# Kernel tuning notes

Hardware: AMD Instinct MI355X
Metric: run time of the kernel (lower is better)

Reference implementation:

```python
import jax, jax.numpy as jnp
import numpy as np

NUM_SKILLS = 1000
DIM_S = 64
SIZE_M = 64
B, T = 64, 200


def setup_inputs() -> dict:
    key = jax.random.key(0)
    ks = jax.random.split(key, 16)
    skills = jax.random.randint(ks[0], (B, T), 0, NUM_SKILLS)
    responses = jax.random.randint(ks[1], (B, T), 0, 2)
    s = 1.0 / np.sqrt(DIM_S)
    return {
        "skills": skills,
        "responses": responses,
        "k_emb": jax.random.normal(ks[2], (NUM_SKILLS, DIM_S)) * s,
        "v_emb": jax.random.normal(ks[3], (2 * NUM_SKILLS, DIM_S)) * s,
        "Mk": jax.random.normal(ks[4], (SIZE_M, DIM_S)) * np.sqrt(2.0 / DIM_S),
        "Mv0": jax.random.normal(ks[5], (SIZE_M, DIM_S)) * np.sqrt(2.0 / DIM_S),
        "fW": jax.random.normal(ks[6], (DIM_S, 2 * DIM_S)) * (1.0 / np.sqrt(2 * DIM_S)),
        "fb": jnp.zeros((DIM_S,)),
        "eW": jax.random.normal(ks[7], (DIM_S, DIM_S)) * s,
        "eb": jnp.zeros((DIM_S,)),
        "aW": jax.random.normal(ks[8], (DIM_S, DIM_S)) * s,
        "ab": jnp.zeros((DIM_S,)),
        "pW": jax.random.normal(ks[9], (1, DIM_S)) * s,
        "pb": jnp.zeros((1,)),
    }


def reference(skills, responses, k_emb, v_emb, Mk, Mv0, fW, fb, eW, eb, aW, ab, pW, pb):
    # dropout is identity in eval mode
    masked_r = responses * (responses > -1).astype(responses.dtype)
    x = skills + NUM_SKILLS * masked_r            # [B, T]
    k = k_emb[skills]                              # [B, T, D]
    v = v_emb[x]                                   # [B, T, D]
    w = jax.nn.softmax(jnp.einsum('btd,md->btm', k, Mk), axis=-1)  # [B, T, M]
    e = jax.nn.sigmoid(v @ eW.T + eb)              # [B, T, D]
    a = jnp.tanh(v @ aW.T + ab)                    # [B, T, D]

    Mv_init = jnp.broadcast_to(Mv0, (skills.shape[0],) + Mv0.shape)  # [B, M, D]

    def step(Mvt, inp):
        wt, et, at = inp                           # [B,M], [B,D], [B,D]
        read = jnp.einsum('bm,bmd->bd', wt, Mvt)   # read BEFORE update (Mv[:, :-1])
        Mvt = Mvt * (1.0 - wt[:, :, None] * et[:, None, :]) + wt[:, :, None] * at[:, None, :]
        return Mvt, read

    xs = (jnp.swapaxes(w, 0, 1), jnp.swapaxes(e, 0, 1), jnp.swapaxes(a, 0, 1))
    _, reads = jax.lax.scan(step, Mv_init, xs)     # reads: [T, B, D]
    reads = jnp.swapaxes(reads, 0, 1)              # [B, T, D]

    f = jnp.tanh(jnp.concatenate([reads, k], axis=-1) @ fW.T + fb)  # [B, T, D]
    p = jax.nn.sigmoid(f @ pW.T + pb)[..., 0]      # [B, T]
    return p[:, 1:]                                # pred, [B, T-1]
```

## Files before the change

### kernel.cpp

```cpp
#include <hip/hip_runtime.h>
#include <hip/hip_bf16.h>
#include <stdint.h>

#define NSK 1000
#define DD 64
#define MM 64
#define BB 64
#define TT 200

__device__ __forceinline__ float lane_bcast(float v, int l) {
  return __uint_as_float(__builtin_amdgcn_readlane(__float_as_uint(v), l));
}

__global__ __launch_bounds__(256) void wea_kernel(
    const int* __restrict__ skills, const int* __restrict__ responses,
    const float* __restrict__ k_emb, const float* __restrict__ v_emb,
    const float* __restrict__ Mk, const float* __restrict__ eW,
    const float* __restrict__ eb, const float* __restrict__ aW,
    const float* __restrict__ ab,
    float* __restrict__ w_ws, float* __restrict__ e_ws, float* __restrict__ a_ws)
{
  __shared__ float sMk[4096], seW[4096], saW[4096];
  const int tid = threadIdx.x;
  for (int Q = tid; Q < 1024; Q += 256) {
    const int j = Q >> 4, c = Q & 15;
    const int dst = j * 64 + ((c + j) & 15) * 4;
    *(float4*)&sMk[dst] = ((const float4*)Mk)[Q];
    *(float4*)&seW[dst] = ((const float4*)eW)[Q];
    *(float4*)&saW[dst] = ((const float4*)aW)[Q];
  }
  __syncthreads();

  const int wave = tid >> 6, lane = tid & 63;
  const float ebl = eb[lane], abl = ab[lane];

  float kvs[4], vvs[4];
  #pragma unroll
  for (int i = 0; i < 4; ++i) {
    const int row = blockIdx.x * 16 + wave * 4 + i;
    const int sk = skills[row];
    int r = responses[row]; r = (r > -1) ? r : 0;
    kvs[i] = k_emb[(size_t)sk * DD + lane];
    vvs[i] = v_emb[(size_t)(sk + NSK * r) * DD + lane];
  }

  #pragma unroll 1
  for (int i = 0; i < 4; ++i) {
    const int row = blockIdx.x * 16 + wave * 4 + i;
    const float kv = kvs[i], vv = vvs[i];

    float accK = 0.f, accE = 0.f, accA = 0.f;
    #pragma unroll
    for (int c = 0; c < 16; ++c) {
      const int off = lane * 64 + ((c + lane) & 15) * 4;
      float4 qm = *(const float4*)&sMk[off];
      float4 qe = *(const float4*)&seW[off];
      float4 qa = *(const float4*)&saW[off];
      float mm[4] = {qm.x, qm.y, qm.z, qm.w};
      float ee[4] = {qe.x, qe.y, qe.z, qe.w};
      float aa[4] = {qa.x, qa.y, qa.z, qa.w};
      #pragma unroll
      for (int j = 0; j < 4; ++j) {
        const int d = c * 4 + j;
        const float kd = lane_bcast(kv, d);
        const float vd = lane_bcast(vv, d);
        accK = fmaf(kd, mm[j], accK);
        accE = fmaf(vd, ee[j], accE);
        accA = fmaf(vd, aa[j], accA);
      }
    }
    float mx = accK;
    #pragma unroll
    for (int off = 32; off; off >>= 1) mx = fmaxf(mx, __shfl_xor(mx, off));
    float ex = __expf(accK - mx);
    float sm = ex;
    #pragma unroll
    for (int off = 32; off; off >>= 1) sm += __shfl_xor(sm, off);
    const float wv  = ex / sm;
    const float evv = 1.f / (1.f + __expf(-(accE + ebl)));
    const float avv = tanhf(accA + abl);
    w_ws[(size_t)row * 64 + lane] = wv;
    e_ws[(size_t)row * 64 + lane] = evv;
    a_ws[(size_t)row * 64 + lane] = avv;
  }
}

#define CH 8

__device__ __forceinline__ void load_chunk(
    const float* __restrict__ wr, const float* __restrict__ er,
    const float* __restrict__ ar, int t0, int wl, int lane,
    float* wb, float* ebf, float* abf)
{
  #pragma unroll
  for (int k = 0; k < CH; ++k) {
    wb[k]  = wr[(t0 + k) * 64 + wl];
    ebf[k] = er[(t0 + k) * 64 + lane];
    abf[k] = ar[(t0 + k) * 64 + lane];
  }
}

__device__ __forceinline__ void compute_chunk(
    float* Mv, const float* wb, const float* ebf, const float* abf,
    int t0, int wave, int lane, float* __restrict__ pr)
{
  #pragma unroll
  for (int k = 0; k < CH; ++k) {
    const float wv = wb[k], ev = ebf[k], av = abf[k];
    float rp = 0.f;
    #pragma unroll
    for (int i = 0; i < 16; ++i) {
      float wm = lane_bcast(wv, i);
      rp = fmaf(wm, Mv[i], rp);
      float tp = fmaf(-ev, Mv[i], av);
      Mv[i] = fmaf(wm, tp, Mv[i]);
    }
    pr[(t0 + k) * 256 + wave * 64 + lane] = rp;
  }
}

__global__ __launch_bounds__(256) void scan_kernel(
    const float* __restrict__ Mv0,
    const float* __restrict__ w_ws, const float* __restrict__ e_ws,
    const float* __restrict__ a_ws, float* __restrict__ part_ws)
{
  const int b    = blockIdx.x;
  const int wave = threadIdx.x >> 6;
  const int lane = threadIdx.x & 63;
  const int m0   = wave * 16;
  const int wl   = m0 + (lane & 15);
  float Mv[16];
  #pragma unroll
  for (int i = 0; i < 16; ++i) Mv[i] = Mv0[(size_t)(m0 + i) * DD + lane];

  const float* wr = w_ws + (size_t)b * TT * 64;
  const float* er = e_ws + (size_t)b * TT * 64;
  const float* ar = a_ws + (size_t)b * TT * 64;
  float* pr = part_ws + (size_t)b * TT * 256;

  float wb0[CH], eb0[CH], ab0[CH];
  float wb1[CH], eb1[CH], ab1[CH];
  load_chunk(wr, er, ar, 0, wl, lane, wb0, eb0, ab0);

  for (int ch = 0; ch < TT / CH; ch += 2) {
    if ((ch + 1) * CH < TT)
      load_chunk(wr, er, ar, (ch + 1) * CH, wl, lane, wb1, eb1, ab1);
    compute_chunk(Mv, wb0, eb0, ab0, ch * CH, wave, lane, pr);
    if ((ch + 2) * CH < TT)
      load_chunk(wr, er, ar, (ch + 2) * CH, wl, lane, wb0, eb0, ab0);
    if ((ch + 1) * CH < TT)
      compute_chunk(Mv, wb1, eb1, ab1, (ch + 1) * CH, wave, lane, pr);
  }
}

__global__ __launch_bounds__(256) void fp_kernel(
    const int* __restrict__ skills, const float* __restrict__ k_emb,
    const float* __restrict__ fW, const float* __restrict__ fb,
    const float* __restrict__ pW, const float* __restrict__ pb,
    const float* __restrict__ part_ws, float* __restrict__ out)
{
  __shared__ float sfW[8192];
  const int tid = threadIdx.x;
  for (int Q = tid; Q < 2048; Q += 256) {
    const int j = Q >> 5, c = Q & 31;
    *(float4*)&sfW[j * 128 + ((c + j) & 31) * 4] = ((const float4*)fW)[Q];
  }
  __syncthreads();

  const int wave = tid >> 6, lane = tid & 63;
  const float fbl = fb[lane];
  const float pwl = pW[lane];
  const float pb0 = pb[0];

  float rvs[4], kvs[4];
  #pragma unroll
  for (int i = 0; i < 4; ++i) {
    const int idx = blockIdx.x * 16 + wave * 4 + i;
    const int b   = idx / (TT - 1);
    const int tm1 = idx % (TT - 1);
    const int row = b * TT + tm1 + 1;
    const float* pp = part_ws + (size_t)row * 256;
    rvs[i] = (pp[lane] + pp[64 + lane]) + (pp[128 + lane] + pp[192 + lane]);
    kvs[i] = k_emb[(size_t)skills[row] * DD + lane];
  }

  #pragma unroll 1
  for (int i = 0; i < 4; ++i) {
    const int idx = blockIdx.x * 16 + wave * 4 + i;
    const int b   = idx / (TT - 1);
    const int tm1 = idx % (TT - 1);
    const float rv = rvs[i], kv = kvs[i];

    float acc = fbl;
    #pragma unroll
    for (int c = 0; c < 32; ++c) {
      const int off = lane * 128 + ((c + lane) & 31) * 4;
      float4 q = *(const float4*)&sfW[off];
      float ww[4] = {q.x, q.y, q.z, q.w};
      #pragma unroll
      for (int j = 0; j < 4; ++j) {
        const int d = c * 4 + j;
        const float s = (d < 64) ? lane_bcast(rv, d) : lane_bcast(kv, d - 64);
        acc = fmaf(s, ww[j], acc);
      }
    }
    float fj = tanhf(acc);
    float prod = fj * pwl;
    #pragma unroll
    for (int off = 32; off; off >>= 1) prod += __shfl_xor(prod, off);
    float p = 1.f / (1.f + __expf(-(prod + pb0)));
    if (lane == 0) out[(size_t)b * (TT - 1) + tm1] = p;
  }
}

extern "C" void kernel_launch(void* const* d_in, const int* in_sizes, int n_in,
                              void* d_out, int out_size, void* d_ws, size_t ws_size,
                              hipStream_t stream) {
  const int* skills    = (const int*)d_in[0];
  const int* responses = (const int*)d_in[1];
  const float* k_emb   = (const float*)d_in[2];
  const float* v_emb   = (const float*)d_in[3];
  const float* Mk      = (const float*)d_in[4];
  const float* Mv0     = (const float*)d_in[5];
  const float* fW      = (const float*)d_in[6];
  const float* fb      = (const float*)d_in[7];
  const float* eW      = (const float*)d_in[8];
  const float* eb      = (const float*)d_in[9];
  const float* aW      = (const float*)d_in[10];
  const float* ab      = (const float*)d_in[11];
  const float* pW      = (const float*)d_in[12];
  const float* pb      = (const float*)d_in[13];

  float* w_ws    = (float*)d_ws;
  float* e_ws    = w_ws + (size_t)BB * TT * 64;
  float* a_ws    = e_ws + (size_t)BB * TT * 64;
  float* part_ws = a_ws + (size_t)BB * TT * 64;

  wea_kernel<<<dim3(BB * TT / 16), 256, 0, stream>>>(
      skills, responses, k_emb, v_emb, Mk, eW, eb, aW, ab, w_ws, e_ws, a_ws);
  scan_kernel<<<dim3(BB), 256, 0, stream>>>(Mv0, w_ws, e_ws, a_ws, part_ws);
  fp_kernel<<<dim3(BB * (TT - 1) / 16), 256, 0, stream>>>(
      skills, k_emb, fW, fb, pW, pb, part_ws, (float*)d_out);
}
```

Baseline: 146.5 us.

## Split scan across two blocks per batch and reuse LDS weight loads across rows

The recurrent scan now runs on 128 blocks, two per batch, each owning 32 memory slots with 8 rows per wave instead of 16. This halves the serial per-step work per wave and doubles the number of CUs in use. The partial-read workspace grows to 8 partials per step, and fp_kernel sums all eight. Both wea_kernel and fp_kernel are also restructured so each LDS weight fragment is loaded once and applied to all 4 rows, reducing LDS traffic at the cost of more live registers. The larger partial buffer adds global write and read traffic.

```diff
diff --git a/kernel.cpp b/kernel.cpp
--- a/kernel.cpp
+++ b/kernel.cpp
@@ -44,48 +44,58 @@
     vvs[i] = v_emb[(size_t)(sk + NSK * r) * DD + lane];
   }
 
+  float accK[4] = {0.f, 0.f, 0.f, 0.f};
+  float accE[4] = {0.f, 0.f, 0.f, 0.f};
+  float accA[4] = {0.f, 0.f, 0.f, 0.f};
   #pragma unroll 1
+  for (int h = 0; h < 4; ++h) {
+    float4 qm[4], qe[4], qa[4];
+    #pragma unroll
+    for (int c = 0; c < 4; ++c) {
+      const int cc = h * 4 + c;
+      const int off = lane * 64 + ((cc + lane) & 15) * 4;
+      qm[c] = *(const float4*)&sMk[off];
+      qe[c] = *(const float4*)&seW[off];
+      qa[c] = *(const float4*)&saW[off];
+    }
+    #pragma unroll
+    for (int i = 0; i < 4; ++i) {
+      #pragma unroll
+      for (int c = 0; c < 4; ++c) {
+        const float mm[4] = {qm[c].x, qm[c].y, qm[c].z, qm[c].w};
+        const float ee[4] = {qe[c].x, qe[c].y, qe[c].z, qe[c].w};
+        const float aa[4] = {qa[c].x, qa[c].y, qa[c].z, qa[c].w};
+        #pragma unroll
+        for (int j = 0; j < 4; ++j) {
+          const int d = (h * 4 + c) * 4 + j;
+          const float kd = lane_bcast(kvs[i], d);
+          const float vd = lane_bcast(vvs[i], d);
+          accK[i] = fmaf(kd, mm[j], accK[i]);
+          accE[i] = fmaf(vd, ee[j], accE[i]);
+          accA[i] = fmaf(vd, aa[j], accA[i]);
+        }
+      }
+    }
+  }
+
+  #pragma unroll
   for (int i = 0; i < 4; ++i) {
     const int row = blockIdx.x * 16 + wave * 4 + i;
-    const float kv = kvs[i], vv = vvs[i];
-
-    float accK = 0.f, accE = 0.f, accA = 0.f;
-    #pragma unroll
-    for (int c = 0; c < 16; ++c) {
-      const int off = lane * 64 + ((c + lane) & 15) * 4;
-      float4 qm = *(const float4*)&sMk[off];
-      float4 qe = *(const float4*)&seW[off];
-      float4 qa = *(const float4*)&saW[off];
-      float mm[4] = {qm.x, qm.y, qm.z, qm.w};
-      float ee[4] = {qe.x, qe.y, qe.z, qe.w};
-      float aa[4] = {qa.x, qa.y, qa.z, qa.w};
-      #pragma unroll
-      for (int j = 0; j < 4; ++j) {
-        const int d = c * 4 + j;
-        const float kd = lane_bcast(kv, d);
-        const float vd = lane_bcast(vv, d);
-        accK = fmaf(kd, mm[j], accK);
-        accE = fmaf(vd, ee[j], accE);
-        accA = fmaf(vd, aa[j], accA);
-      }
-    }
-    float mx = accK;
+    float mx = accK[i];
     #pragma unroll
     for (int off = 32; off; off >>= 1) mx = fmaxf(mx, __shfl_xor(mx, off));
-    float ex = __expf(accK - mx);
+    float ex = __expf(accK[i] - mx);
     float sm = ex;
     #pragma unroll
     for (int off = 32; off; off >>= 1) sm += __shfl_xor(sm, off);
-    const float wv  = ex / sm;
-    const float evv = 1.f / (1.f + __expf(-(accE + ebl)));
-    const float avv = tanhf(accA + abl);
-    w_ws[(size_t)row * 64 + lane] = wv;
-    e_ws[(size_t)row * 64 + lane] = evv;
-    a_ws[(size_t)row * 64 + lane] = avv;
+    w_ws[(size_t)row * 64 + lane] = ex / sm;
+    e_ws[(size_t)row * 64 + lane] = 1.f / (1.f + __expf(-(accE[i] + ebl)));
+    a_ws[(size_t)row * 64 + lane] = tanhf(accA[i] + abl);
   }
 }
 
 #define CH 8
+#define RW 8
 
 __device__ __forceinline__ void load_chunk(
     const float* __restrict__ wr, const float* __restrict__ er,
@@ -102,20 +112,20 @@
 
 __device__ __forceinline__ void compute_chunk(
     float* Mv, const float* wb, const float* ebf, const float* abf,
-    int t0, int wave, int lane, float* __restrict__ pr)
+    int t0, int part, int lane, float* __restrict__ pr)
 {
   #pragma unroll
   for (int k = 0; k < CH; ++k) {
     const float wv = wb[k], ev = ebf[k], av = abf[k];
     float rp = 0.f;
     #pragma unroll
-    for (int i = 0; i < 16; ++i) {
+    for (int i = 0; i < RW; ++i) {
       float wm = lane_bcast(wv, i);
       rp = fmaf(wm, Mv[i], rp);
       float tp = fmaf(-ev, Mv[i], av);
       Mv[i] = fmaf(wm, tp, Mv[i]);
     }
-    pr[(t0 + k) * 256 + wave * 64 + lane] = rp;
+    pr[(t0 + k) * 512 + part * 64 + lane] = rp;
   }
 }
 
@@ -124,19 +134,21 @@
     const float* __restrict__ w_ws, const float* __restrict__ e_ws,
     const float* __restrict__ a_ws, float* __restrict__ part_ws)
 {
-  const int b    = blockIdx.x;
+  const int b    = blockIdx.x >> 1;
+  const int s    = blockIdx.x & 1;
   const int wave = threadIdx.x >> 6;
   const int lane = threadIdx.x & 63;
-  const int m0   = wave * 16;
-  const int wl   = m0 + (lane & 15);
-  float Mv[16];
-  #pragma unroll
-  for (int i = 0; i < 16; ++i) Mv[i] = Mv0[(size_t)(m0 + i) * DD + lane];
+  const int m0   = s * 32 + wave * RW;
+  const int part = s * 4 + wave;
+  const int wl   = m0 + (lane & (RW - 1));
+  float Mv[RW];
+  #pragma unroll
+  for (int i = 0; i < RW; ++i) Mv[i] = Mv0[(size_t)(m0 + i) * DD + lane];
 
   const float* wr = w_ws + (size_t)b * TT * 64;
   const float* er = e_ws + (size_t)b * TT * 64;
   const float* ar = a_ws + (size_t)b * TT * 64;
-  float* pr = part_ws + (size_t)b * TT * 256;
+  float* pr = part_ws + (size_t)b * TT * 512;
 
   float wb0[CH], eb0[CH], ab0[CH];
   float wb1[CH], eb1[CH], ab1[CH];
@@ -145,11 +157,11 @@
   for (int ch = 0; ch < TT / CH; ch += 2) {
     if ((ch + 1) * CH < TT)
       load_chunk(wr, er, ar, (ch + 1) * CH, wl, lane, wb1, eb1, ab1);
-    compute_chunk(Mv, wb0, eb0, ab0, ch * CH, wave, lane, pr);
+    compute_chunk(Mv, wb0, eb0, ab0, ch * CH, part, lane, pr);
     if ((ch + 2) * CH < TT)
       load_chunk(wr, er, ar, (ch + 2) * CH, wl, lane, wb0, eb0, ab0);
     if ((ch + 1) * CH < TT)
-      compute_chunk(Mv, wb1, eb1, ab1, (ch + 1) * CH, wave, lane, pr);
+      compute_chunk(Mv, wb1, eb1, ab1, (ch + 1) * CH, part, lane, pr);
   }
 }
 
@@ -179,32 +191,45 @@
     const int b   = idx / (TT - 1);
     const int tm1 = idx % (TT - 1);
     const int row = b * TT + tm1 + 1;
-    const float* pp = part_ws + (size_t)row * 256;
-    rvs[i] = (pp[lane] + pp[64 + lane]) + (pp[128 + lane] + pp[192 + lane]);
+    const float* pp = part_ws + (size_t)row * 512;
+    float r0 = pp[lane]       + pp[64 + lane];
+    float r1 = pp[128 + lane] + pp[192 + lane];
+    float r2 = pp[256 + lane] + pp[320 + lane];
+    float r3 = pp[384 + lane] + pp[448 + lane];
+    rvs[i] = (r0 + r1) + (r2 + r3);
     kvs[i] = k_emb[(size_t)skills[row] * DD + lane];
   }
 
+  float acc[4] = {fbl, fbl, fbl, fbl};
   #pragma unroll 1
+  for (int h = 0; h < 4; ++h) {
+    float4 qf[8];
+    #pragma unroll
+    for (int c = 0; c < 8; ++c) {
+      const int cc = h * 8 + c;
+      qf[c] = *(const float4*)&sfW[lane * 128 + ((cc + lane) & 31) * 4];
+    }
+    #pragma unroll
+    for (int i = 0; i < 4; ++i) {
+      #pragma unroll
+      for (int c = 0; c < 8; ++c) {
+        const float ww[4] = {qf[c].x, qf[c].y, qf[c].z, qf[c].w};
+        #pragma unroll
+        for (int j = 0; j < 4; ++j) {
+          const int d = (h * 8 + c) * 4 + j;
+          const float sv = (d < 64) ? lane_bcast(rvs[i], d) : lane_bcast(kvs[i], d - 64);
+          acc[i] = fmaf(sv, ww[j], acc[i]);
+        }
+      }
+    }
+  }
+
+  #pragma unroll
   for (int i = 0; i < 4; ++i) {
     const int idx = blockIdx.x * 16 + wave * 4 + i;
     const int b   = idx / (TT - 1);
     const int tm1 = idx % (TT - 1);
-    const float rv = rvs[i], kv = kvs[i];
-
-    float acc = fbl;
-    #pragma unroll
-    for (int c = 0; c < 32; ++c) {
-      const int off = lane * 128 + ((c + lane) & 31) * 4;
-      float4 q = *(const float4*)&sfW[off];
-      float ww[4] = {q.x, q.y, q.z, q.w};
-      #pragma unroll
-      for (int j = 0; j < 4; ++j) {
-        const int d = c * 4 + j;
-        const float s = (d < 64) ? lane_bcast(rv, d) : lane_bcast(kv, d - 64);
-        acc = fmaf(s, ww[j], acc);
-      }
-    }
-    float fj = tanhf(acc);
+    float fj = tanhf(acc[i]);
     float prod = fj * pwl;
     #pragma unroll
     for (int off = 32; off; off >>= 1) prod += __shfl_xor(prod, off);
@@ -238,7 +263,7 @@
 
   wea_kernel<<<dim3(BB * TT / 16), 256, 0, stream>>>(
       skills, responses, k_emb, v_emb, Mk, eW, eb, aW, ab, w_ws, e_ws, a_ws);
-  scan_kernel<<<dim3(BB), 256, 0, stream>>>(Mv0, w_ws, e_ws, a_ws, part_ws);
+  scan_kernel<<<dim3(BB * 2), 256, 0, stream>>>(Mv0, w_ws, e_ws, a_ws, part_ws);
   fp_kernel<<<dim3(BB * (TT - 1) / 16), 256, 0, stream>>>(
       skills, k_emb, fW, fb, pW, pb, part_ws, (float*)d_out);
 }
```

After: 153.1 us. 1.04x slower.
